# Performance work log

Hardware: AMD Instinct MI355X
Metric: run time of the kernel (lower is better)

## Reference

```python
import jax, jax.numpy as jnp
import numpy as np

B, T, D, N = 256, 512, 512, 64


def setup_inputs() -> dict:
    key = jax.random.key(0)
    ks = jax.random.split(key, 8)
    s = 0.05  # keep gate pre-activations in a sane range
    return {
        "x": jax.random.normal(ks[0], (B, T, D), dtype=jnp.float32),
        "init_h": jax.random.normal(ks[1], (B, D), dtype=jnp.float32) * s,
        "W_ih": jax.random.normal(ks[2], (4 * D, D + N), dtype=jnp.float32) * s,
        "b_ih": jax.random.normal(ks[3], (4 * D,), dtype=jnp.float32) * s,
        "W_hh": jax.random.normal(ks[4], (4 * D, D), dtype=jnp.float32) * s,
        "b_hh": jax.random.normal(ks[5], (4 * D,), dtype=jnp.float32) * s,
        "W_lin": jax.random.normal(ks[6], (N, D), dtype=jnp.float32) * s,
        "b_lin": jax.random.normal(ks[7], (N,), dtype=jnp.float32) * s,
    }


def reference(x, init_h, W_ih, b_ih, W_hh, b_hh, W_lin, b_lin):
    n_class = W_lin.shape[0]
    d = init_h.shape[-1]

    def step(carry, x_t):
        h, c, y = carry
        inp = jnp.concatenate([x_t, y], axis=-1)  # [B, D+N]
        gates = inp @ W_ih.T + b_ih + h @ W_hh.T + b_hh  # [B, 4D]
        i, f, g, o = jnp.split(gates, 4, axis=-1)
        i = jax.nn.sigmoid(i)
        f = jax.nn.sigmoid(f)
        g = jnp.tanh(g)
        o = jax.nn.sigmoid(o)
        c = f * c + i * g
        h = o * jnp.tanh(c)
        y = jax.nn.softmax(h @ W_lin.T + b_lin, axis=-1)  # [B, N]
        return (h, c, y), y

    c0 = jnp.zeros_like(init_h)
    y0 = jnp.zeros((x.shape[0], n_class), dtype=x.dtype)
    xs = jnp.swapaxes(x, 0, 1)  # [T, B, D]
    _, ys = jax.lax.scan(step, (init_h, c0, y0), xs)  # ys: [T, B, N]
    return jnp.swapaxes(ys, 0, 1)  # [B, T, N]
```

## Files before the change

kernel.cpp:

```cpp
#include <hip/hip_runtime.h>
#include <cstdint>
#include <cstddef>


typedef _Float16 f16x8 __attribute__((ext_vector_type(8)));
typedef float f32x4 __attribute__((ext_vector_type(4)));

#define MFMA16(a, b, c_) __builtin_amdgcn_mfma_f32_16x16x32_f16((a), (b), (c_), 0, 0, 0)
#define AGT __HIP_MEMORY_SCOPE_AGENT
#define RLX __ATOMIC_RELAXED

#define FLAG_INTS (256 * 64 + 64)
#define HS2_U32 131072

static __device__ __forceinline__ unsigned short f2b(_Float16 h) {
  return __builtin_bit_cast(unsigned short, h);
}
static __device__ __forceinline__ _Float16 b2f(unsigned short s) {
  return __builtin_bit_cast(_Float16, s);
}

__device__ __forceinline__ void cvt8(const float4 a, const float4 b, f16x8& hi, f16x8& lo) {
  float v[8] = {a.x, a.y, a.z, a.w, b.x, b.y, b.z, b.w};
#pragma unroll
  for (int j = 0; j < 8; ++j) {
    _Float16 h = (_Float16)v[j];
    hi[j] = h;
    lo[j] = (_Float16)(v[j] - (float)h);
  }
}

template <bool XPRE>
__global__ void prep_kernel(const float* __restrict__ x, const float* __restrict__ init_h,
                            const float* __restrict__ W_ih, const float* __restrict__ b_ih,
                            const float* __restrict__ W_hh, const float* __restrict__ b_hh,
                            _Float16* __restrict__ xs, _Float16* __restrict__ wf,
                            unsigned int* __restrict__ hs2, float* __restrict__ bias,
                            int* __restrict__ flags) {
  const long NX = XPRE ? 256L * 512 * 16 * 4 : 0;
  const int NWF = 128 * 34 * 64;
  const int NH2 = 256 * 16 * 4;
  long tid = (long)blockIdx.x * 256 + threadIdx.x;

  if (XPRE && tid < NX) {
    int q = tid & 3, ki = (tid >> 2) & 15, t = (tid >> 6) & 511;
    int row = (int)(tid >> 15);
    const float* s = x + (((size_t)row * 512 + t) * 512 + ki * 32 + 4 * q);
    float4 a = *(const float4*)s, b = *(const float4*)(s + 16);
    f16x8 hi, lo;
    cvt8(a, b, hi, lo);
    _Float16* d = xs + ((((size_t)row * 512 + t) * 16 + ki) * 64 + q * 16);
    *(f16x8*)d = hi;
    *(f16x8*)(d + 8) = lo;
    return;
  }
  long u = tid - NX;
  if (u >= 0 && u < NWF) {
    int l = (int)(u & 63);
    int u2 = (int)(u >> 6);
    int ki = u2 % 34, ct = u2 / 34;
    int cb = ct >> 1, cth = ct & 1;
    int l15 = l & 15;
    int col = (l15 >> 2) * 512 + cb * 8 + cth * 4 + (l15 & 3);
    int k = ki * 32 + 4 * (l >> 4);
    float4 a, b;
    if (k < 512) {
      const float* p = W_ih + (size_t)col * 576;
      a = *(const float4*)(p + k);
      b = *(const float4*)(p + k + 16);
    } else if (k < 1024) {
      const float* p = W_hh + (size_t)col * 512;
      a = *(const float4*)(p + k - 512);
      b = *(const float4*)(p + k - 512 + 16);
    } else {
      const float* p = W_ih + (size_t)col * 576 + 512;
      a = *(const float4*)(p + k - 1024);
      b = *(const float4*)(p + k - 1024 + 16);
    }
    f16x8 hi, lo;
    cvt8(a, b, hi, lo);
    _Float16* d = wf + (((size_t)ct * 34 + ki) * 64 + l) * 16;
    *(f16x8*)d = hi;
    *(f16x8*)(d + 8) = lo;
    return;
  }
  u -= NWF;
  if (u >= 0 && u < NH2) {
    int q = (int)(u & 3), ki = (int)((u >> 2) & 15), row = (int)(u >> 6);
    const float* s = init_h + ((size_t)row * 512 + ki * 32 + 4 * q);
    float4 a = *(const float4*)s, b = *(const float4*)(s + 16);
    float v[8] = {a.x, a.y, a.z, a.w, b.x, b.y, b.z, b.w};
    unsigned int pk[8];
#pragma unroll
    for (int j = 0; j < 8; ++j) {
      _Float16 hh = (_Float16)v[j];
      _Float16 hl = (_Float16)(v[j] - (float)hh);
      pk[j] = (unsigned int)f2b(hh) | ((unsigned int)f2b(hl) << 16);
    }
    unsigned int* base = hs2 + ((size_t)row * 16 + ki) * 32;
    *(uint4*)(base + 4 * q) = make_uint4(pk[0], pk[1], pk[2], pk[3]);
    *(uint4*)(base + 16 + 4 * q) = make_uint4(pk[4], pk[5], pk[6], pk[7]);
    return;
  }
  u -= NH2;
  if (u >= 0 && u < 2048) {
    bias[u] = b_ih[u] + b_hh[u];
    return;
  }
  u -= 2048;
  if (u >= 0 && u < FLAG_INTS) flags[u] = 0;
}

#define GKSTEP(AH, AL, KI)                                                       \
  {                                                                              \
    const f16x8 b0h = *(const f16x8*)(wfl_hi + ((size_t)(KI)*64 + l) * 8);       \
    const f16x8 b1h = *(const f16x8*)(wfl_hi + 17408 + ((size_t)(KI)*64 + l) * 8); \
    const f16x8 b0l = *(const f16x8*)(wfl_lo + ((size_t)(KI)*64 + l) * 8);       \
    const f16x8 b1l = *(const f16x8*)(wfl_lo + 17408 + ((size_t)(KI)*64 + l) * 8); \
    aC0 = MFMA16((AH), b0h, aC0);                                                \
    aC1 = MFMA16((AH), b1h, aC1);                                                \
    aC0 = MFMA16((AL), b0h, aC0);                                                \
    aC1 = MFMA16((AL), b1h, aC1);                                                \
    aC0 = MFMA16((AH), b0l, aC0);                                                \
    aC1 = MFMA16((AH), b1l, aC1);                                                \
  }

template <bool XPRE>
__global__ void __launch_bounds__(512, 2) recur_kernel(
    const float* __restrict__ x, const float* __restrict__ b_lin,
    const float* __restrict__ W_lin, const _Float16* __restrict__ xs,
    const _Float16* __restrict__ wf, unsigned int* __restrict__ hs2,
    const float* __restrict__ bias, float* __restrict__ out, float* __restrict__ ylog,
    int* __restrict__ flags) {
  const int bid = blockIdx.x;
  const int x8 = bid & 7;
  const int g = x8 >> 1;
  const int cb = (x8 & 1) * 32 + (bid >> 3);
  const int tid = threadIdx.x;
  const int l = tid & 63, w = tid >> 6;
  const int l15 = l & 15, q = l >> 4;
  const int kh = w & 1, rtp = w >> 1;

  __shared__ _Float16 wfl_hi[2 * 34 * 64 * 8];
  __shared__ _Float16 wfl_lo[2 * 34 * 64 * 8];
  __shared__ float pacc[4][2][4][64];
  __shared__ float lp[4][16];
  __shared__ int s_ab;

  {
    const _Float16* srcw = wf + (size_t)cb * 4352 * 16;
#pragma unroll
    for (int i = 0; i < 9; ++i) {
      int u = tid + i * 512;
      if (u < 4352) {
        const float4* s16 = (const float4*)(srcw + (size_t)u * 16);
        *(float4*)(wfl_hi + (size_t)u * 8) = s16[0];
        *(float4*)(wfl_lo + (size_t)u * 8) = s16[1];
      }
    }
    if (tid == 0) s_ab = 0;
  }
  __syncthreads();

  const int dd = l15 & 3, rr = l15 >> 2;
  float bg[2][4];
#pragma unroll
  for (int c2 = 0; c2 < 2; ++c2)
#pragma unroll
    for (int gi = 0; gi < 4; ++gi) bg[c2][gi] = bias[gi * 512 + cb * 8 + c2 * 4 + dd];
  const float blin = b_lin[cb];

  const int Rw = g * 64 + rtp * 16;
  const int rowA = Rw + l15;
  const int hoff = rowA * 512 + 4 * q;
  const _Float16* xsA = xs + (size_t)rowA * 524288 + q * 16;
  const float* xfA = x + (size_t)rowA * 262144 + 4 * q;
  const float* wl = W_lin + (size_t)cb * 512;

  const int rowE = Rw + 4 * q + rr;
  unsigned int hwo[2];
#pragma unroll
  for (int c2 = 0; c2 < 2; ++c2) {
    int dglob = cb * 8 + c2 * 4 + dd;
    int kiH = dglob >> 5, k32 = dglob & 31;
    int e = 4 * ((k32 & 15) >> 2) + (k32 & 3) + 16 * (k32 >> 4);
    hwo[c2] = (unsigned int)((rowE * 16 + kiH) * 32 + e);
  }

  int* abortf = flags + 256 * 64;

  auto ARRIVE = [&](int v) {
    __syncthreads();
    if (tid == 0) __hip_atomic_store(flags + (size_t)(g * 64 + cb) * 64, v, RLX, AGT);
  };
  auto WAIT = [&](int v) -> bool {
    if (tid < 64) {
      int a = 0;
      int* f = flags + ((size_t)g * 64 + tid) * 64;
      int it = 0;
      while (__hip_atomic_load(f, RLX, AGT) < v) {
        __builtin_amdgcn_s_sleep(1);
        if (++it > 400000) {
          a = 1;
          break;
        }
        if ((it & 255) == 0 && __hip_atomic_load(abortf, RLX, AGT) != 0) {
          a = 1;
          break;
        }
      }
      a = __any(a) ? 1 : 0;
      if (tid == 0) {
        if (a) __hip_atomic_store(abortf, 1, RLX, AGT);
        s_ab = a;
      }
    }
    __syncthreads();
    return s_ab != 0;
  };

  float cst[2] = {0.f, 0.f};
  f32x4 aC0, aC1;

#pragma unroll 1
  for (int s = 0; s < 512; ++s) {
    aC0 = (f32x4){0.f, 0.f, 0.f, 0.f};
    aC1 = (f32x4){0.f, 0.f, 0.f, 0.f};

    if (XPRE) {
      const _Float16* xA = xsA + (size_t)s * 1024;
#pragma unroll
      for (int i = 0; i < 8; ++i) {
        int kx = kh * 8 + i;
        f16x8 ah = *(const f16x8*)(xA + kx * 64);
        f16x8 al = *(const f16x8*)(xA + kx * 64 + 8);
        GKSTEP(ah, al, kx);
      }
    } else {
      const float* xp = xfA + (size_t)s * 512;
#pragma unroll 2
      for (int i = 0; i < 8; ++i) {
        int kx = kh * 8 + i;
        float4 av = *(const float4*)(xp + kx * 32);
        float4 bv = *(const float4*)(xp + kx * 32 + 16);
        f16x8 ah, al;
        cvt8(av, bv, ah, al);
        GKSTEP(ah, al, kx);
      }
    }

    if (s > 0) {
      if (WAIT(2 * s)) return;
    }

    const unsigned int* hp0 = hs2 + (size_t)(s & 1) * HS2_U32 + hoff;
    f16x8 hh[8], hl[8];
#pragma unroll
    for (int i = 0; i < 8; ++i) {
      const unsigned int* hp = hp0 + (kh * 8 + i) * 32;
      unsigned long long u0 = __hip_atomic_load((const unsigned long long*)hp, RLX, AGT);
      unsigned long long u1 = __hip_atomic_load((const unsigned long long*)(hp + 2), RLX, AGT);
      unsigned long long u2 = __hip_atomic_load((const unsigned long long*)(hp + 16), RLX, AGT);
      unsigned long long u3 = __hip_atomic_load((const unsigned long long*)(hp + 18), RLX, AGT);
      unsigned int wd[8] = {(unsigned int)u0, (unsigned int)(u0 >> 32),
                            (unsigned int)u1, (unsigned int)(u1 >> 32),
                            (unsigned int)u2, (unsigned int)(u2 >> 32),
                            (unsigned int)u3, (unsigned int)(u3 >> 32)};
#pragma unroll
      for (int j = 0; j < 8; ++j) {
        hh[i][j] = b2f((unsigned short)(wd[j] & 0xffffu));
        hl[i][j] = b2f((unsigned short)(wd[j] >> 16));
      }
    }

    float dlg = 0.f;
#pragma unroll
    for (int i = 0; i < 8; ++i) {
      int kk = kh * 8 + i;
      float4 wa = *(const float4*)(wl + kk * 32 + 4 * q);
      float4 wb2 = *(const float4*)(wl + kk * 32 + 16 + 4 * q);
      dlg += ((float)hh[i][0] + (float)hl[i][0]) * wa.x +
             ((float)hh[i][1] + (float)hl[i][1]) * wa.y +
             ((float)hh[i][2] + (float)hl[i][2]) * wa.z +
             ((float)hh[i][3] + (float)hl[i][3]) * wa.w +
             ((float)hh[i][4] + (float)hl[i][4]) * wb2.x +
             ((float)hh[i][5] + (float)hl[i][5]) * wb2.y +
             ((float)hh[i][6] + (float)hl[i][6]) * wb2.z +
             ((float)hh[i][7] + (float)hl[i][7]) * wb2.w;
    }
    dlg += __shfl_xor(dlg, 16);
    dlg += __shfl_xor(dlg, 32);
    if (kh == 1 && l < 16) lp[rtp][l15] = dlg;
    __syncthreads();
    if (kh == 0 && l < 16) {
      float full = dlg + lp[rtp][l15] + blin;
      __hip_atomic_store(ylog + ((size_t)g * 64 + cb) * 64 + rtp * 16 + l15, full, RLX, AGT);
    }
    ARRIVE(2 * s + 1);

#pragma unroll
    for (int i = 0; i < 8; ++i) GKSTEP(hh[i], hl[i], 16 + kh * 8 + i);

    if (WAIT(2 * s + 1)) return;

    if (s > 0) {
      float la[4][4];
#pragma unroll
      for (int b2 = 0; b2 < 4; ++b2)
#pragma unroll
        for (int m = 0; m < 4; ++m)
          la[b2][m] = __hip_atomic_load(
              ylog + ((size_t)g * 64 + 16 * b2 + 4 * q + m) * 64 + rtp * 16 + l15, RLX, AGT);
      float mx = la[0][0];
#pragma unroll
      for (int b2 = 0; b2 < 4; ++b2)
#pragma unroll
        for (int m = 0; m < 4; ++m) mx = fmaxf(mx, la[b2][m]);
      mx = fmaxf(mx, __shfl_xor(mx, 16));
      mx = fmaxf(mx, __shfl_xor(mx, 32));
      float sm = 0.f;
#pragma unroll
      for (int b2 = 0; b2 < 4; ++b2)
#pragma unroll
        for (int m = 0; m < 4; ++m) {
          la[b2][m] = __expf(la[b2][m] - mx);
          sm += la[b2][m];
        }
      sm += __shfl_xor(sm, 16);
      sm += __shfl_xor(sm, 32);
      float inv = 1.f / sm;
      if (cb == 0 && kh == 0) {
        size_t ob = (((size_t)(g * 64 + rtp * 16 + l15)) * 512 + (s - 1)) * 64;
#pragma unroll
        for (int b2 = 0; b2 < 4; ++b2)
#pragma unroll
          for (int m = 0; m < 4; ++m) out[ob + 16 * b2 + 4 * q + m] = la[b2][m] * inv;
      }
      f16x8 yh;
      if (kh == 0) {
#pragma unroll
        for (int j = 0; j < 8; ++j) yh[j] = (_Float16)(la[j >> 2][j & 3] * inv);
      } else {
#pragma unroll
        for (int j = 0; j < 8; ++j) yh[j] = (_Float16)(la[(j >> 2) + 2][j & 3] * inv);
      }
      const int KY = 32 + kh;
      const f16x8 b0h = *(const f16x8*)(wfl_hi + ((size_t)KY * 64 + l) * 8);
      const f16x8 b1h = *(const f16x8*)(wfl_hi + 17408 + ((size_t)KY * 64 + l) * 8);
      const f16x8 b0l = *(const f16x8*)(wfl_lo + ((size_t)KY * 64 + l) * 8);
      const f16x8 b1l = *(const f16x8*)(wfl_lo + 17408 + ((size_t)KY * 64 + l) * 8);
      aC0 = MFMA16(yh, b0h, aC0);
      aC1 = MFMA16(yh, b1h, aC1);
      aC0 = MFMA16(yh, b0l, aC0);
      aC1 = MFMA16(yh, b1l, aC1);
    }

    if (kh == 1) {
#pragma unroll
      for (int r = 0; r < 4; ++r) {
        pacc[rtp][0][r][l] = aC0[r];
        pacc[rtp][1][r][l] = aC1[r];
      }
    }
    __syncthreads();
    if (kh == 0) {
#pragma unroll
      for (int r = 0; r < 4; ++r) {
        aC0[r] += pacc[rtp][0][r][l];
        aC1[r] += pacc[rtp][1][r][l];
      }
      const unsigned int wb_ = (unsigned int)(((s & 1) ^ 1) * HS2_U32);
#pragma unroll
      for (int c2 = 0; c2 < 2; ++c2) {
        f32x4 A = c2 ? aC1 : aC0;
        float z[4];
#pragma unroll
        for (int gi = 0; gi < 4; ++gi) {
          int src = (l & 48) | (gi * 4 + dd);
          float v0 = __shfl(A[0], src), v1 = __shfl(A[1], src);
          float v2 = __shfl(A[2], src), v3 = __shfl(A[3], src);
          z[gi] = (rr == 0) ? v0 : (rr == 1) ? v1 : (rr == 2) ? v2 : v3;
        }
        float zi = z[0] + bg[c2][0], zf = z[1] + bg[c2][1];
        float zg = z[2] + bg[c2][2], zo = z[3] + bg[c2][3];
        float iv = 1.f / (1.f + __expf(-zi));
        float fv = 1.f / (1.f + __expf(-zf));
        float eg = __expf(2.f * zg);
        float gv = 1.f - 2.f / (eg + 1.f);
        float ov = 1.f / (1.f + __expf(-zo));
        float cn = fv * cst[c2] + iv * gv;
        cst[c2] = cn;
        float ec = __expf(2.f * cn);
        float th = 1.f - 2.f / (ec + 1.f);
        float hv = ov * th;
        _Float16 hh2 = (_Float16)hv;
        _Float16 hl2 = (_Float16)(hv - (float)hh2);
        unsigned int pk = (unsigned int)f2b(hh2) | ((unsigned int)f2b(hl2) << 16);
        __hip_atomic_store(hs2 + wb_ + hwo[c2], pk, RLX, AGT);
      }
    }
    ARRIVE(2 * s + 2);
  }

  if (WAIT(1024)) return;
  {
    const unsigned int* hp0 = hs2 + hoff;
    float dlg = 0.f;
#pragma unroll
    for (int i = 0; i < 8; ++i) {
      int kk = kh * 8 + i;
      const unsigned int* hp = hp0 + kk * 32;
      unsigned long long u0 = __hip_atomic_load((const unsigned long long*)hp, RLX, AGT);
      unsigned long long u1 = __hip_atomic_load((const unsigned long long*)(hp + 2), RLX, AGT);
      unsigned long long u2 = __hip_atomic_load((const unsigned long long*)(hp + 16), RLX, AGT);
      unsigned long long u3 = __hip_atomic_load((const unsigned long long*)(hp + 18), RLX, AGT);
      unsigned int wd[8] = {(unsigned int)u0, (unsigned int)(u0 >> 32),
                            (unsigned int)u1, (unsigned int)(u1 >> 32),
                            (unsigned int)u2, (unsigned int)(u2 >> 32),
                            (unsigned int)u3, (unsigned int)(u3 >> 32)};
      float4 wa = *(const float4*)(wl + kk * 32 + 4 * q);
      float4 wb2 = *(const float4*)(wl + kk * 32 + 16 + 4 * q);
      float hv0[8];
#pragma unroll
      for (int j = 0; j < 8; ++j)
        hv0[j] = (float)b2f((unsigned short)(wd[j] & 0xffffu)) +
                 (float)b2f((unsigned short)(wd[j] >> 16));
      dlg += hv0[0] * wa.x + hv0[1] * wa.y + hv0[2] * wa.z + hv0[3] * wa.w + hv0[4] * wb2.x +
             hv0[5] * wb2.y + hv0[6] * wb2.z + hv0[7] * wb2.w;
    }
    dlg += __shfl_xor(dlg, 16);
    dlg += __shfl_xor(dlg, 32);
    if (kh == 1 && l < 16) lp[rtp][l15] = dlg;
    __syncthreads();
    if (kh == 0 && l < 16)
      __hip_atomic_store(ylog + ((size_t)g * 64 + cb) * 64 + rtp * 16 + l15,
                         dlg + lp[rtp][l15] + blin, RLX, AGT);
  }
  ARRIVE(1025);
  if (WAIT(1025)) return;
  if (cb == 0 && kh == 0) {
    float la[4][4];
#pragma unroll
    for (int b2 = 0; b2 < 4; ++b2)
#pragma unroll
      for (int m = 0; m < 4; ++m)
        la[b2][m] = __hip_atomic_load(
            ylog + ((size_t)g * 64 + 16 * b2 + 4 * q + m) * 64 + rtp * 16 + l15, RLX, AGT);
    float mx = la[0][0];
#pragma unroll
    for (int b2 = 0; b2 < 4; ++b2)
#pragma unroll
      for (int m = 0; m < 4; ++m) mx = fmaxf(mx, la[b2][m]);
    mx = fmaxf(mx, __shfl_xor(mx, 16));
    mx = fmaxf(mx, __shfl_xor(mx, 32));
    float sm = 0.f;
#pragma unroll
    for (int b2 = 0; b2 < 4; ++b2)
#pragma unroll
      for (int m = 0; m < 4; ++m) {
        la[b2][m] = __expf(la[b2][m] - mx);
        sm += la[b2][m];
      }
    sm += __shfl_xor(sm, 16);
    sm += __shfl_xor(sm, 32);
    float inv = 1.f / sm;
    size_t ob = (((size_t)(g * 64 + rtp * 16 + l15)) * 512 + 511) * 64;
#pragma unroll
    for (int b2 = 0; b2 < 4; ++b2)
#pragma unroll
      for (int m = 0; m < 4; ++m) out[ob + 16 * b2 + 4 * q + m] = la[b2][m] * inv;
  }
}

extern "C" void kernel_launch(void* const* d_in, const int* in_sizes, int n_in, void* d_out,
                              int out_size, void* d_ws, size_t ws_size, hipStream_t stream) {
  const float* x = (const float*)d_in[0];
  const float* init_h = (const float*)d_in[1];
  const float* W_ih = (const float*)d_in[2];
  const float* b_ih = (const float*)d_in[3];
  const float* W_hh = (const float*)d_in[4];
  const float* b_hh = (const float*)d_in[5];
  const float* W_lin = (const float*)d_in[6];
  const float* b_lin = (const float*)d_in[7];
  float* out = (float*)d_out;
  (void)in_sizes;
  (void)n_in;
  (void)out_size;

  char* ws = (char*)d_ws;
  size_t off = 0;
  auto take = [&](size_t bytes) -> char* {
    char* r = ws + off;
    off = (off + bytes + 255) & ~(size_t)255;
    return r;
  };
  const size_t WF_E = (size_t)128 * 34 * 64 * 16;
  const size_t XS_E = (size_t)256 * 512 * 16 * 64;

  _Float16* wf = (_Float16*)take(WF_E * 2);
  unsigned int* hs2 = (unsigned int*)take((size_t)2 * HS2_U32 * 4);
  float* bias = (float*)take(2048 * 4);
  float* ylogb = (float*)take((size_t)4 * 64 * 64 * 4);
  int* flags = (int*)take((size_t)FLAG_INTS * 4);
  if (ws_size < off) return;
  _Float16* xs = (_Float16*)(ws + off);
  const bool xpre = (ws_size >= off + XS_E * 2);

  if (xpre) {
    const long total = 8388608L + 278528 + 16384 + 2048 + FLAG_INTS;
    prep_kernel<true><<<(int)((total + 255) / 256), 256, 0, stream>>>(
        x, init_h, W_ih, b_ih, W_hh, b_hh, xs, wf, hs2, bias, flags);
    recur_kernel<true><<<256, 512, 0, stream>>>(x, b_lin, W_lin, xs, wf, hs2, bias, out, ylogb,
                                                flags);
  } else {
    const long total = 278528L + 16384 + 2048 + FLAG_INTS;
    prep_kernel<false><<<(int)((total + 255) / 256), 256, 0, stream>>>(
        x, init_h, W_ih, b_ih, W_hh, b_hh, xs, wf, hs2, bias, flags);
    recur_kernel<false><<<256, 512, 0, stream>>>(x, b_lin, W_lin, xs, wf, hs2, bias, out, ylogb,
                                                 flags);
  }
}
```

Before: 8.857 ms.

## Compute output logits redundantly per block via MFMA, halving grid barriers per step

Each block now computes the full 64-class logit projection and softmax for its rows with MFMA, using an hi/lo fp16 copy of W_lin kept in LDS. This removes the second cross-block barrier and the shared logit buffer per timestep. The gate weights are no longer staged in LDS and are read from global memory instead. The x-projection for the next step is issued after the arrive so it can overlap the barrier wait. In exchange the linear layer is computed redundantly in every column block, and all gate-weight traffic now goes through the global cache.

```diff
diff --git a/kernel.cpp b/kernel.cpp
--- a/kernel.cpp
+++ b/kernel.cpp
@@ -5,6 +5,7 @@
 
 typedef _Float16 f16x8 __attribute__((ext_vector_type(8)));
 typedef float f32x4 __attribute__((ext_vector_type(4)));
+typedef unsigned long long u64;
 
 #define MFMA16(a, b, c_) __builtin_amdgcn_mfma_f32_16x16x32_f16((a), (b), (c_), 0, 0, 0)
 #define AGT __HIP_MEMORY_SCOPE_AGENT
@@ -34,12 +35,14 @@
 __global__ void prep_kernel(const float* __restrict__ x, const float* __restrict__ init_h,
                             const float* __restrict__ W_ih, const float* __restrict__ b_ih,
                             const float* __restrict__ W_hh, const float* __restrict__ b_hh,
-                            _Float16* __restrict__ xs, _Float16* __restrict__ wf,
-                            unsigned int* __restrict__ hs2, float* __restrict__ bias,
-                            int* __restrict__ flags) {
+                            const float* __restrict__ W_lin, _Float16* __restrict__ xs,
+                            _Float16* __restrict__ wf, _Float16* __restrict__ wlf_hi,
+                            _Float16* __restrict__ wlf_lo, unsigned int* __restrict__ hs2,
+                            float* __restrict__ bias, int* __restrict__ flags) {
   const long NX = XPRE ? 256L * 512 * 16 * 4 : 0;
   const int NWF = 128 * 34 * 64;
-  const int NH2 = 256 * 16 * 4;
+  const int NWLF = 4 * 16 * 64;
+  const int NH2 = 256 * 128;
   long tid = (long)blockIdx.x * 256 + threadIdx.x;
 
   if (XPRE && tid < NX) {
@@ -85,21 +88,35 @@
     return;
   }
   u -= NWF;
+  if (u >= 0 && u < NWLF) {
+    int l = (int)(u & 63);
+    int u2 = (int)(u >> 6);
+    int ki = u2 & 15, ct = u2 >> 4;
+    int col = ct * 16 + (l & 15);
+    int k = ki * 32 + 4 * (l >> 4);
+    const float* p = W_lin + (size_t)col * 512;
+    float4 a = *(const float4*)(p + k), b = *(const float4*)(p + k + 16);
+    f16x8 hi, lo;
+    cvt8(a, b, hi, lo);
+    _Float16* dh = wlf_hi + ((size_t)(ct * 16 + ki) * 64 + l) * 8;
+    _Float16* dl = wlf_lo + ((size_t)(ct * 16 + ki) * 64 + l) * 8;
+    *(f16x8*)dh = hi;
+    *(f16x8*)dl = lo;
+    return;
+  }
+  u -= NWLF;
   if (u >= 0 && u < NH2) {
-    int q = (int)(u & 3), ki = (int)((u >> 2) & 15), row = (int)(u >> 6);
-    const float* s = init_h + ((size_t)row * 512 + ki * 32 + 4 * q);
-    float4 a = *(const float4*)s, b = *(const float4*)(s + 16);
-    float v[8] = {a.x, a.y, a.z, a.w, b.x, b.y, b.z, b.w};
-    unsigned int pk[8];
-#pragma unroll
-    for (int j = 0; j < 8; ++j) {
+    int g4 = (int)(u & 127), row = (int)(u >> 7);
+    const float* s = init_h + (size_t)row * 512 + g4 * 4;
+    float4 a = *(const float4*)s;
+    float v[4] = {a.x, a.y, a.z, a.w};
+    unsigned int* d = hs2 + (size_t)row * 512 + g4 * 4;
+#pragma unroll
+    for (int j = 0; j < 4; ++j) {
       _Float16 hh = (_Float16)v[j];
       _Float16 hl = (_Float16)(v[j] - (float)hh);
-      pk[j] = (unsigned int)f2b(hh) | ((unsigned int)f2b(hl) << 16);
-    }
-    unsigned int* base = hs2 + ((size_t)row * 16 + ki) * 32;
-    *(uint4*)(base + 4 * q) = make_uint4(pk[0], pk[1], pk[2], pk[3]);
-    *(uint4*)(base + 16 + 4 * q) = make_uint4(pk[4], pk[5], pk[6], pk[7]);
+      d[j] = (unsigned int)f2b(hh) | ((unsigned int)f2b(hl) << 16);
+    }
     return;
   }
   u -= NH2;
@@ -111,26 +128,12 @@
   if (u >= 0 && u < FLAG_INTS) flags[u] = 0;
 }
 
-#define GKSTEP(AH, AL, KI)                                                       \
-  {                                                                              \
-    const f16x8 b0h = *(const f16x8*)(wfl_hi + ((size_t)(KI)*64 + l) * 8);       \
-    const f16x8 b1h = *(const f16x8*)(wfl_hi + 17408 + ((size_t)(KI)*64 + l) * 8); \
-    const f16x8 b0l = *(const f16x8*)(wfl_lo + ((size_t)(KI)*64 + l) * 8);       \
-    const f16x8 b1l = *(const f16x8*)(wfl_lo + 17408 + ((size_t)(KI)*64 + l) * 8); \
-    aC0 = MFMA16((AH), b0h, aC0);                                                \
-    aC1 = MFMA16((AH), b1h, aC1);                                                \
-    aC0 = MFMA16((AL), b0h, aC0);                                                \
-    aC1 = MFMA16((AL), b1h, aC1);                                                \
-    aC0 = MFMA16((AH), b0l, aC0);                                                \
-    aC1 = MFMA16((AH), b1l, aC1);                                                \
-  }
-
 template <bool XPRE>
-__global__ void __launch_bounds__(512, 2) recur_kernel(
+__global__ void __launch_bounds__(512, 1) recur_kernel(
     const float* __restrict__ x, const float* __restrict__ b_lin,
-    const float* __restrict__ W_lin, const _Float16* __restrict__ xs,
-    const _Float16* __restrict__ wf, unsigned int* __restrict__ hs2,
-    const float* __restrict__ bias, float* __restrict__ out, float* __restrict__ ylog,
+    const _Float16* __restrict__ xs, const _Float16* __restrict__ wf,
+    const _Float16* __restrict__ wlf_hi, const _Float16* __restrict__ wlf_lo,
+    unsigned int* __restrict__ hs2, const float* __restrict__ bias, float* __restrict__ out,
     int* __restrict__ flags) {
   const int bid = blockIdx.x;
   const int x8 = bid & 7;
@@ -141,22 +144,17 @@
   const int l15 = l & 15, q = l >> 4;
   const int kh = w & 1, rtp = w >> 1;
 
-  __shared__ _Float16 wfl_hi[2 * 34 * 64 * 8];
-  __shared__ _Float16 wfl_lo[2 * 34 * 64 * 8];
-  __shared__ float pacc[4][2][4][64];
-  __shared__ float lp[4][16];
+  __shared__ _Float16 wlin_h[4 * 16 * 64 * 8];
+  __shared__ _Float16 wlin_l[4 * 16 * 64 * 8];
+  __shared__ float scratch[4608];
   __shared__ int s_ab;
 
   {
-    const _Float16* srcw = wf + (size_t)cb * 4352 * 16;
-#pragma unroll
-    for (int i = 0; i < 9; ++i) {
+#pragma unroll
+    for (int i = 0; i < 8; ++i) {
       int u = tid + i * 512;
-      if (u < 4352) {
-        const float4* s16 = (const float4*)(srcw + (size_t)u * 16);
-        *(float4*)(wfl_hi + (size_t)u * 8) = s16[0];
-        *(float4*)(wfl_lo + (size_t)u * 8) = s16[1];
-      }
+      *(float4*)(wlin_h + (size_t)u * 8) = *(const float4*)(wlf_hi + (size_t)u * 8);
+      *(float4*)(wlin_l + (size_t)u * 8) = *(const float4*)(wlf_lo + (size_t)u * 8);
     }
     if (tid == 0) s_ab = 0;
   }
@@ -168,24 +166,17 @@
   for (int c2 = 0; c2 < 2; ++c2)
 #pragma unroll
     for (int gi = 0; gi < 4; ++gi) bg[c2][gi] = bias[gi * 512 + cb * 8 + c2 * 4 + dd];
-  const float blin = b_lin[cb];
+  const float blv0 = b_lin[l15], blv1 = b_lin[16 + l15];
+  const float blv2 = b_lin[32 + l15], blv3 = b_lin[48 + l15];
 
   const int Rw = g * 64 + rtp * 16;
   const int rowA = Rw + l15;
-  const int hoff = rowA * 512 + 4 * q;
   const _Float16* xsA = xs + (size_t)rowA * 524288 + q * 16;
   const float* xfA = x + (size_t)rowA * 262144 + 4 * q;
-  const float* wl = W_lin + (size_t)cb * 512;
-
+  const unsigned int* hldA = hs2 + (size_t)rowA * 512 + 4 * q;
   const int rowE = Rw + 4 * q + rr;
-  unsigned int hwo[2];
-#pragma unroll
-  for (int c2 = 0; c2 < 2; ++c2) {
-    int dglob = cb * 8 + c2 * 4 + dd;
-    int kiH = dglob >> 5, k32 = dglob & 31;
-    int e = 4 * ((k32 & 15) >> 2) + (k32 & 3) + 16 * (k32 >> 4);
-    hwo[c2] = (unsigned int)((rowE * 16 + kiH) * 32 + e);
-  }
+
+  const _Float16* wfb = wf + ((size_t)(2 * cb) * 34) * 1024 + (size_t)l * 16;
 
   int* abortf = flags + 256 * 64;
 
@@ -219,25 +210,30 @@
     return s_ab != 0;
   };
 
-  float cst[2] = {0.f, 0.f};
-  f32x4 aC0, aC1;
-
-#pragma unroll 1
-  for (int s = 0; s < 512; ++s) {
-    aC0 = (f32x4){0.f, 0.f, 0.f, 0.f};
-    aC1 = (f32x4){0.f, 0.f, 0.f, 0.f};
-
+  auto GK3 = [&](const f16x8& ah, const f16x8& al, int KI, f32x4& A0, f32x4& A1) {
+    const _Float16* p0 = wfb + (size_t)KI * 1024;
+    const _Float16* p1 = p0 + 34 * 1024;
+    f16x8 b0h = *(const f16x8*)p0, b0l = *(const f16x8*)(p0 + 8);
+    f16x8 b1h = *(const f16x8*)p1, b1l = *(const f16x8*)(p1 + 8);
+    A0 = MFMA16(ah, b0h, A0);
+    A1 = MFMA16(ah, b1h, A1);
+    A0 = MFMA16(al, b0h, A0);
+    A1 = MFMA16(al, b1h, A1);
+    A0 = MFMA16(ah, b0l, A0);
+    A1 = MFMA16(ah, b1l, A1);
+  };
+  auto XGEMM = [&](int t, f32x4& A0, f32x4& A1) {
     if (XPRE) {
-      const _Float16* xA = xsA + (size_t)s * 1024;
+      const _Float16* xA = xsA + (size_t)t * 1024;
 #pragma unroll
       for (int i = 0; i < 8; ++i) {
         int kx = kh * 8 + i;
         f16x8 ah = *(const f16x8*)(xA + kx * 64);
         f16x8 al = *(const f16x8*)(xA + kx * 64 + 8);
-        GKSTEP(ah, al, kx);
+        GK3(ah, al, kx, A0, A1);
       }
     } else {
-      const float* xp = xfA + (size_t)s * 512;
+      const float* xp = xfA + (size_t)t * 512;
 #pragma unroll 2
       for (int i = 0; i < 8; ++i) {
         int kx = kh * 8 + i;
@@ -245,23 +241,31 @@
         float4 bv = *(const float4*)(xp + kx * 32 + 16);
         f16x8 ah, al;
         cvt8(av, bv, ah, al);
-        GKSTEP(ah, al, kx);
-      }
-    }
-
+        GK3(ah, al, kx, A0, A1);
+      }
+    }
+  };
+
+  const f32x4 Z = {0.f, 0.f, 0.f, 0.f};
+  float cst[2] = {0.f, 0.f};
+  f32x4 aC0 = Z, aC1 = Z;
+  XGEMM(0, aC0, aC1);
+
+#pragma unroll 1
+  for (int s = 0; s < 512; ++s) {
     if (s > 0) {
-      if (WAIT(2 * s)) return;
-    }
-
-    const unsigned int* hp0 = hs2 + (size_t)(s & 1) * HS2_U32 + hoff;
+      if (WAIT(s)) return;
+    }
+
     f16x8 hh[8], hl[8];
+    const unsigned int* hp0 = hldA + (size_t)(s & 1) * HS2_U32;
 #pragma unroll
     for (int i = 0; i < 8; ++i) {
       const unsigned int* hp = hp0 + (kh * 8 + i) * 32;
-      unsigned long long u0 = __hip_atomic_load((const unsigned long long*)hp, RLX, AGT);
-      unsigned long long u1 = __hip_atomic_load((const unsigned long long*)(hp + 2), RLX, AGT);
-      unsigned long long u2 = __hip_atomic_load((const unsigned long long*)(hp + 16), RLX, AGT);
-      unsigned long long u3 = __hip_atomic_load((const unsigned long long*)(hp + 18), RLX, AGT);
+      u64 u0 = __hip_atomic_load((const u64*)hp, RLX, AGT);
+      u64 u1 = __hip_atomic_load((const u64*)(hp + 2), RLX, AGT);
+      u64 u2 = __hip_atomic_load((const u64*)(hp + 16), RLX, AGT);
+      u64 u3 = __hip_atomic_load((const u64*)(hp + 18), RLX, AGT);
       unsigned int wd[8] = {(unsigned int)u0, (unsigned int)(u0 >> 32),
                             (unsigned int)u1, (unsigned int)(u1 >> 32),
                             (unsigned int)u2, (unsigned int)(u2 >> 32),
@@ -273,103 +277,137 @@
       }
     }
 
-    float dlg = 0.f;
-#pragma unroll
-    for (int i = 0; i < 8; ++i) {
-      int kk = kh * 8 + i;
-      float4 wa = *(const float4*)(wl + kk * 32 + 4 * q);
-      float4 wb2 = *(const float4*)(wl + kk * 32 + 16 + 4 * q);
-      dlg += ((float)hh[i][0] + (float)hl[i][0]) * wa.x +
-             ((float)hh[i][1] + (float)hl[i][1]) * wa.y +
-             ((float)hh[i][2] + (float)hl[i][2]) * wa.z +
-             ((float)hh[i][3] + (float)hl[i][3]) * wa.w +
-             ((float)hh[i][4] + (float)hl[i][4]) * wb2.x +
-             ((float)hh[i][5] + (float)hl[i][5]) * wb2.y +
-             ((float)hh[i][6] + (float)hl[i][6]) * wb2.z +
-             ((float)hh[i][7] + (float)hl[i][7]) * wb2.w;
-    }
-    dlg += __shfl_xor(dlg, 16);
-    dlg += __shfl_xor(dlg, 32);
-    if (kh == 1 && l < 16) lp[rtp][l15] = dlg;
-    __syncthreads();
-    if (kh == 0 && l < 16) {
-      float full = dlg + lp[rtp][l15] + blin;
-      __hip_atomic_store(ylog + ((size_t)g * 64 + cb) * 64 + rtp * 16 + l15, full, RLX, AGT);
-    }
-    ARRIVE(2 * s + 1);
-
-#pragma unroll
-    for (int i = 0; i < 8; ++i) GKSTEP(hh[i], hl[i], 16 + kh * 8 + i);
-
-    if (WAIT(2 * s + 1)) return;
-
+    f32x4 y0 = Z, y1 = Z, y2 = Z, y3 = Z;
     if (s > 0) {
-      float la[4][4];
-#pragma unroll
-      for (int b2 = 0; b2 < 4; ++b2)
-#pragma unroll
-        for (int m = 0; m < 4; ++m)
-          la[b2][m] = __hip_atomic_load(
-              ylog + ((size_t)g * 64 + 16 * b2 + 4 * q + m) * 64 + rtp * 16 + l15, RLX, AGT);
-      float mx = la[0][0];
-#pragma unroll
-      for (int b2 = 0; b2 < 4; ++b2)
-#pragma unroll
-        for (int m = 0; m < 4; ++m) mx = fmaxf(mx, la[b2][m]);
-      mx = fmaxf(mx, __shfl_xor(mx, 16));
-      mx = fmaxf(mx, __shfl_xor(mx, 32));
-      float sm = 0.f;
-#pragma unroll
-      for (int b2 = 0; b2 < 4; ++b2)
-#pragma unroll
-        for (int m = 0; m < 4; ++m) {
-          la[b2][m] = __expf(la[b2][m] - mx);
-          sm += la[b2][m];
-        }
-      sm += __shfl_xor(sm, 16);
-      sm += __shfl_xor(sm, 32);
-      float inv = 1.f / sm;
-      if (cb == 0 && kh == 0) {
-        size_t ob = (((size_t)(g * 64 + rtp * 16 + l15)) * 512 + (s - 1)) * 64;
-#pragma unroll
-        for (int b2 = 0; b2 < 4; ++b2)
-#pragma unroll
-          for (int m = 0; m < 4; ++m) out[ob + 16 * b2 + 4 * q + m] = la[b2][m] * inv;
-      }
-      f16x8 yh;
+#pragma unroll
+      for (int i = 0; i < 8; ++i) {
+        int ki = kh * 8 + i;
+        const _Float16* ph0 = wlin_h + ((size_t)(0 * 16 + ki) * 64 + l) * 8;
+        const _Float16* ph1 = wlin_h + ((size_t)(1 * 16 + ki) * 64 + l) * 8;
+        const _Float16* ph2 = wlin_h + ((size_t)(2 * 16 + ki) * 64 + l) * 8;
+        const _Float16* ph3 = wlin_h + ((size_t)(3 * 16 + ki) * 64 + l) * 8;
+        f16x8 b0 = *(const f16x8*)ph0, b1 = *(const f16x8*)ph1;
+        f16x8 b2 = *(const f16x8*)ph2, b3 = *(const f16x8*)ph3;
+        y0 = MFMA16(hh[i], b0, y0);
+        y1 = MFMA16(hh[i], b1, y1);
+        y2 = MFMA16(hh[i], b2, y2);
+        y3 = MFMA16(hh[i], b3, y3);
+        y0 = MFMA16(hl[i], b0, y0);
+        y1 = MFMA16(hl[i], b1, y1);
+        y2 = MFMA16(hl[i], b2, y2);
+        y3 = MFMA16(hl[i], b3, y3);
+        const _Float16* pl0 = wlin_l + ((size_t)(0 * 16 + ki) * 64 + l) * 8;
+        const _Float16* pl1 = wlin_l + ((size_t)(1 * 16 + ki) * 64 + l) * 8;
+        const _Float16* pl2 = wlin_l + ((size_t)(2 * 16 + ki) * 64 + l) * 8;
+        const _Float16* pl3 = wlin_l + ((size_t)(3 * 16 + ki) * 64 + l) * 8;
+        f16x8 c0 = *(const f16x8*)pl0, c1 = *(const f16x8*)pl1;
+        f16x8 c2v = *(const f16x8*)pl2, c3 = *(const f16x8*)pl3;
+        y0 = MFMA16(hh[i], c0, y0);
+        y1 = MFMA16(hh[i], c1, y1);
+        y2 = MFMA16(hh[i], c2v, y2);
+        y3 = MFMA16(hh[i], c3, y3);
+      }
+    }
+#pragma unroll
+    for (int i = 0; i < 8; ++i) GK3(hh[i], hl[i], 16 + kh * 8 + i, aC0, aC1);
+
+    if (s > 0) {
+      if (kh == 1) {
+#pragma unroll
+        for (int r = 0; r < 4; ++r) {
+          scratch[((rtp * 4 + 0) * 4 + r) * 64 + l] = y0[r];
+          scratch[((rtp * 4 + 1) * 4 + r) * 64 + l] = y1[r];
+          scratch[((rtp * 4 + 2) * 4 + r) * 64 + l] = y2[r];
+          scratch[((rtp * 4 + 3) * 4 + r) * 64 + l] = y3[r];
+        }
+      }
+      __syncthreads();
+      float la0[4], la1[4], la2[4], la3[4];
       if (kh == 0) {
 #pragma unroll
-        for (int j = 0; j < 8; ++j) yh[j] = (_Float16)(la[j >> 2][j & 3] * inv);
-      } else {
-#pragma unroll
-        for (int j = 0; j < 8; ++j) yh[j] = (_Float16)(la[(j >> 2) + 2][j & 3] * inv);
-      }
-      const int KY = 32 + kh;
-      const f16x8 b0h = *(const f16x8*)(wfl_hi + ((size_t)KY * 64 + l) * 8);
-      const f16x8 b1h = *(const f16x8*)(wfl_hi + 17408 + ((size_t)KY * 64 + l) * 8);
-      const f16x8 b0l = *(const f16x8*)(wfl_lo + ((size_t)KY * 64 + l) * 8);
-      const f16x8 b1l = *(const f16x8*)(wfl_lo + 17408 + ((size_t)KY * 64 + l) * 8);
-      aC0 = MFMA16(yh, b0h, aC0);
-      aC1 = MFMA16(yh, b1h, aC1);
-      aC0 = MFMA16(yh, b0l, aC0);
-      aC1 = MFMA16(yh, b1l, aC1);
+        for (int r = 0; r < 4; ++r) {
+          la0[r] = y0[r] + scratch[((rtp * 4 + 0) * 4 + r) * 64 + l] + blv0;
+          la1[r] = y1[r] + scratch[((rtp * 4 + 1) * 4 + r) * 64 + l] + blv1;
+          la2[r] = y2[r] + scratch[((rtp * 4 + 2) * 4 + r) * 64 + l] + blv2;
+          la3[r] = y3[r] + scratch[((rtp * 4 + 3) * 4 + r) * 64 + l] + blv3;
+        }
+#pragma unroll
+        for (int r = 0; r < 4; ++r) {
+          float mx = fmaxf(fmaxf(la0[r], la1[r]), fmaxf(la2[r], la3[r]));
+          mx = fmaxf(mx, __shfl_xor(mx, 1));
+          mx = fmaxf(mx, __shfl_xor(mx, 2));
+          mx = fmaxf(mx, __shfl_xor(mx, 4));
+          mx = fmaxf(mx, __shfl_xor(mx, 8));
+          float e0 = __expf(la0[r] - mx), e1 = __expf(la1[r] - mx);
+          float e2 = __expf(la2[r] - mx), e3 = __expf(la3[r] - mx);
+          float sm = e0 + e1 + e2 + e3;
+          sm += __shfl_xor(sm, 1);
+          sm += __shfl_xor(sm, 2);
+          sm += __shfl_xor(sm, 4);
+          sm += __shfl_xor(sm, 8);
+          float inv = 1.f / sm;
+          la0[r] = e0 * inv;
+          la1[r] = e1 * inv;
+          la2[r] = e2 * inv;
+          la3[r] = e3 * inv;
+        }
+        if (cb == 0) {
+#pragma unroll
+          for (int r = 0; r < 4; ++r) {
+            size_t ob = ((size_t)(g * 64 + rtp * 16 + 4 * q + r) * 512 + (s - 1)) * 64 + l15;
+            out[ob] = la0[r];
+            out[ob + 16] = la1[r];
+            out[ob + 32] = la2[r];
+            out[ob + 48] = la3[r];
+          }
+        }
+      }
+      __syncthreads();
+      if (kh == 0) {
+        _Float16* yt = (_Float16*)scratch;
+#pragma unroll
+        for (int r = 0; r < 4; ++r) {
+          int row = rtp * 16 + 4 * q + r;
+          float v[4] = {la0[r], la1[r], la2[r], la3[r]};
+#pragma unroll
+          for (int ct = 0; ct < 4; ++ct) {
+            _Float16 vh = (_Float16)v[ct];
+            _Float16 vl = (_Float16)(v[ct] - (float)vh);
+            yt[row * 136 + ct * 16 + l15] = vh;
+            yt[row * 136 + 72 + ct * 16 + l15] = vl;
+          }
+        }
+      }
+      __syncthreads();
+      {
+        const _Float16* yt = (const _Float16*)scratch + (rtp * 16 + l15) * 136 + kh * 32 + 4 * q;
+        union {
+          u64 d[2];
+          f16x8 v;
+        } th, tl;
+        th.d[0] = *(const u64*)yt;
+        th.d[1] = *(const u64*)(yt + 16);
+        tl.d[0] = *(const u64*)(yt + 72);
+        tl.d[1] = *(const u64*)(yt + 88);
+        GK3(th.v, tl.v, 32 + kh, aC0, aC1);
+      }
+      __syncthreads();
     }
 
     if (kh == 1) {
 #pragma unroll
       for (int r = 0; r < 4; ++r) {
-        pacc[rtp][0][r][l] = aC0[r];
-        pacc[rtp][1][r][l] = aC1[r];
+        scratch[((rtp * 2 + 0) * 4 + r) * 64 + l] = aC0[r];
+        scratch[((rtp * 2 + 1) * 4 + r) * 64 + l] = aC1[r];
       }
     }
     __syncthreads();
     if (kh == 0) {
 #pragma unroll
       for (int r = 0; r < 4; ++r) {
-        aC0[r] += pacc[rtp][0][r][l];
-        aC1[r] += pacc[rtp][1][r][l];
-      }
-      const unsigned int wb_ = (unsigned int)(((s & 1) ^ 1) * HS2_U32);
+        aC0[r] += scratch[((rtp * 2 + 0) * 4 + r) * 64 + l];
+        aC1[r] += scratch[((rtp * 2 + 1) * 4 + r) * 64 + l];
+      }
 #pragma unroll
       for (int c2 = 0; c2 < 2; ++c2) {
         f32x4 A = c2 ? aC1 : aC0;
@@ -391,84 +429,117 @@
         float cn = fv * cst[c2] + iv * gv;
         cst[c2] = cn;
         float ec = __expf(2.f * cn);
-        float th = 1.f - 2.f / (ec + 1.f);
-        float hv = ov * th;
-        _Float16 hh2 = (_Float16)hv;
-        _Float16 hl2 = (_Float16)(hv - (float)hh2);
-        unsigned int pk = (unsigned int)f2b(hh2) | ((unsigned int)f2b(hl2) << 16);
-        __hip_atomic_store(hs2 + wb_ + hwo[c2], pk, RLX, AGT);
-      }
-    }
-    ARRIVE(2 * s + 2);
-  }
-
-  if (WAIT(1024)) return;
+        float th2 = 1.f - 2.f / (ec + 1.f);
+        float hv = ov * th2;
+        _Float16 hhv = (_Float16)hv;
+        _Float16 hlv = (_Float16)(hv - (float)hhv);
+        unsigned int pk = (unsigned int)f2b(hhv) | ((unsigned int)f2b(hlv) << 16);
+        int dglob = cb * 8 + c2 * 4 + dd;
+        __hip_atomic_store(hs2 + (size_t)((s + 1) & 1) * HS2_U32 + rowE * 512 + dglob, pk, RLX,
+                           AGT);
+      }
+    }
+    ARRIVE(s + 1);
+    if (s < 511) {
+      f32x4 aN0 = Z, aN1 = Z;
+      XGEMM(s + 1, aN0, aN1);
+      aC0 = aN0;
+      aC1 = aN1;
+    }
+  }
+
+  if (cb != 0) return;
+  if (WAIT(512)) return;
   {
-    const unsigned int* hp0 = hs2 + hoff;
-    float dlg = 0.f;
+    f16x8 hh[8], hl[8];
+    const unsigned int* hp0 = hldA;
 #pragma unroll
     for (int i = 0; i < 8; ++i) {
-      int kk = kh * 8 + i;
-      const unsigned int* hp = hp0 + kk * 32;
-      unsigned long long u0 = __hip_atomic_load((const unsigned long long*)hp, RLX, AGT);
-      unsigned long long u1 = __hip_atomic_load((const unsigned long long*)(hp + 2), RLX, AGT);
-      unsigned long long u2 = __hip_atomic_load((const unsigned long long*)(hp + 16), RLX, AGT);
-      unsigned long long u3 = __hip_atomic_load((const unsigned long long*)(hp + 18), RLX, AGT);
+      const unsigned int* hp = hp0 + (kh * 8 + i) * 32;
+      u64 u0 = __hip_atomic_load((const u64*)hp, RLX, AGT);
+      u64 u1 = __hip_atomic_load((const u64*)(hp + 2), RLX, AGT);
+      u64 u2 = __hip_atomic_load((const u64*)(hp + 16), RLX, AGT);
+      u64 u3 = __hip_atomic_load((const u64*)(hp + 18), RLX, AGT);
       unsigned int wd[8] = {(unsigned int)u0, (unsigned int)(u0 >> 32),
                             (unsigned int)u1, (unsigned int)(u1 >> 32),
                             (unsigned int)u2, (unsigned int)(u2 >> 32),
                             (unsigned int)u3, (unsigned int)(u3 >> 32)};
-      float4 wa = *(const float4*)(wl + kk * 32 + 4 * q);
-      float4 wb2 = *(const float4*)(wl + kk * 32 + 16 + 4 * q);
-      float hv0[8];
-#pragma unroll
-      for (int j = 0; j < 8; ++j)
-        hv0[j] = (float)b2f((unsigned short)(wd[j] & 0xffffu)) +
-                 (float)b2f((unsigned short)(wd[j] >> 16));
-      dlg += hv0[0] * wa.x + hv0[1] * wa.y + hv0[2] * wa.z + hv0[3] * wa.w + hv0[4] * wb2.x +
-             hv0[5] * wb2.y + hv0[6] * wb2.z + hv0[7] * wb2.w;
-    }
-    dlg += __shfl_xor(dlg, 16);
-    dlg += __shfl_xor(dlg, 32);
-    if (kh == 1 && l < 16) lp[rtp][l15] = dlg;
+#pragma unroll
+      for (int j = 0; j < 8; ++j) {
+        hh[i][j] = b2f((unsigned short)(wd[j] & 0xffffu));
+        hl[i][j] = b2f((unsigned short)(wd[j] >> 16));
+      }
+    }
+    f32x4 y0 = Z, y1 = Z, y2 = Z, y3 = Z;
+#pragma unroll
+    for (int i = 0; i < 8; ++i) {
+      int ki = kh * 8 + i;
+      const _Float16* ph0 = wlin_h + ((size_t)(0 * 16 + ki) * 64 + l) * 8;
+      const _Float16* ph1 = wlin_h + ((size_t)(1 * 16 + ki) * 64 + l) * 8;
+      const _Float16* ph2 = wlin_h + ((size_t)(2 * 16 + ki) * 64 + l) * 8;
+      const _Float16* ph3 = wlin_h + ((size_t)(3 * 16 + ki) * 64 + l) * 8;
+      f16x8 b0 = *(const f16x8*)ph0, b1 = *(const f16x8*)ph1;
+      f16x8 b2 = *(const f16x8*)ph2, b3 = *(const f16x8*)ph3;
+      y0 = MFMA16(hh[i], b0, y0);
+      y1 = MFMA16(hh[i], b1, y1);
+      y2 = MFMA16(hh[i], b2, y2);
+      y3 = MFMA16(hh[i], b3, y3);
+      y0 = MFMA16(hl[i], b0, y0);
+      y1 = MFMA16(hl[i], b1, y1);
+      y2 = MFMA16(hl[i], b2, y2);
+      y3 = MFMA16(hl[i], b3, y3);
+      const _Float16* pl0 = wlin_l + ((size_t)(0 * 16 + ki) * 64 + l) * 8;
+      const _Float16* pl1 = wlin_l + ((size_t)(1 * 16 + ki) * 64 + l) * 8;
+      const _Float16* pl2 = wlin_l + ((size_t)(2 * 16 + ki) * 64 + l) * 8;
+      const _Float16* pl3 = wlin_l + ((size_t)(3 * 16 + ki) * 64 + l) * 8;
+      f16x8 c0 = *(const f16x8*)pl0, c1 = *(const f16x8*)pl1;
+      f16x8 c2v = *(const f16x8*)pl2, c3 = *(const f16x8*)pl3;
+      y0 = MFMA16(hh[i], c0, y0);
+      y1 = MFMA16(hh[i], c1, y1);
+      y2 = MFMA16(hh[i], c2v, y2);
+      y3 = MFMA16(hh[i], c3, y3);
+    }
+    if (kh == 1) {
+#pragma unroll
+      for (int r = 0; r < 4; ++r) {
+        scratch[((rtp * 4 + 0) * 4 + r) * 64 + l] = y0[r];
+        scratch[((rtp * 4 + 1) * 4 + r) * 64 + l] = y1[r];
+        scratch[((rtp * 4 + 2) * 4 + r) * 64 + l] = y2[r];
+        scratch[((rtp * 4 + 3) * 4 + r) * 64 + l] = y3[r];
+      }
+    }
     __syncthreads();
-    if (kh == 0 && l < 16)
-      __hip_atomic_store(ylog + ((size_t)g * 64 + cb) * 64 + rtp * 16 + l15,
-                         dlg + lp[rtp][l15] + blin, RLX, AGT);
-  }
-  ARRIVE(1025);
-  if (WAIT(1025)) return;
-  if (cb == 0 && kh == 0) {
-    float la[4][4];
-#pragma unroll
-    for (int b2 = 0; b2 < 4; ++b2)
-#pragma unroll
-      for (int m = 0; m < 4; ++m)
-        la[b2][m] = __hip_atomic_load(
-            ylog + ((size_t)g * 64 + 16 * b2 + 4 * q + m) * 64 + rtp * 16 + l15, RLX, AGT);
-    float mx = la[0][0];
-#pragma unroll
-    for (int b2 = 0; b2 < 4; ++b2)
-#pragma unroll
-      for (int m = 0; m < 4; ++m) mx = fmaxf(mx, la[b2][m]);
-    mx = fmaxf(mx, __shfl_xor(mx, 16));
-    mx = fmaxf(mx, __shfl_xor(mx, 32));
-    float sm = 0.f;
-#pragma unroll
-    for (int b2 = 0; b2 < 4; ++b2)
-#pragma unroll
-      for (int m = 0; m < 4; ++m) {
-        la[b2][m] = __expf(la[b2][m] - mx);
-        sm += la[b2][m];
-      }
-    sm += __shfl_xor(sm, 16);
-    sm += __shfl_xor(sm, 32);
-    float inv = 1.f / sm;
-    size_t ob = (((size_t)(g * 64 + rtp * 16 + l15)) * 512 + 511) * 64;
-#pragma unroll
-    for (int b2 = 0; b2 < 4; ++b2)
-#pragma unroll
-      for (int m = 0; m < 4; ++m) out[ob + 16 * b2 + 4 * q + m] = la[b2][m] * inv;
+    if (kh == 0) {
+      float la0[4], la1[4], la2[4], la3[4];
+#pragma unroll
+      for (int r = 0; r < 4; ++r) {
+        la0[r] = y0[r] + scratch[((rtp * 4 + 0) * 4 + r) * 64 + l] + blv0;
+        la1[r] = y1[r] + scratch[((rtp * 4 + 1) * 4 + r) * 64 + l] + blv1;
+        la2[r] = y2[r] + scratch[((rtp * 4 + 2) * 4 + r) * 64 + l] + blv2;
+        la3[r] = y3[r] + scratch[((rtp * 4 + 3) * 4 + r) * 64 + l] + blv3;
+      }
+#pragma unroll
+      for (int r = 0; r < 4; ++r) {
+        float mx = fmaxf(fmaxf(la0[r], la1[r]), fmaxf(la2[r], la3[r]));
+        mx = fmaxf(mx, __shfl_xor(mx, 1));
+        mx = fmaxf(mx, __shfl_xor(mx, 2));
+        mx = fmaxf(mx, __shfl_xor(mx, 4));
+        mx = fmaxf(mx, __shfl_xor(mx, 8));
+        float e0 = __expf(la0[r] - mx), e1 = __expf(la1[r] - mx);
+        float e2 = __expf(la2[r] - mx), e3 = __expf(la3[r] - mx);
+        float sm = e0 + e1 + e2 + e3;
+        sm += __shfl_xor(sm, 1);
+        sm += __shfl_xor(sm, 2);
+        sm += __shfl_xor(sm, 4);
+        sm += __shfl_xor(sm, 8);
+        float inv = 1.f / sm;
+        size_t ob = ((size_t)(g * 64 + rtp * 16 + 4 * q + r) * 512 + 511) * 64 + l15;
+        out[ob] = e0 * inv;
+        out[ob + 16] = e1 * inv;
+        out[ob + 32] = e2 * inv;
+        out[ob + 48] = e3 * inv;
+      }
+    }
   }
 }
 
@@ -495,28 +566,30 @@
     return r;
   };
   const size_t WF_E = (size_t)128 * 34 * 64 * 16;
+  const size_t WLF_E = (size_t)4 * 16 * 64 * 8;
   const size_t XS_E = (size_t)256 * 512 * 16 * 64;
 
   _Float16* wf = (_Float16*)take(WF_E * 2);
+  _Float16* wlf_hi = (_Float16*)take(WLF_E * 2);
+  _Float16* wlf_lo = (_Float16*)take(WLF_E * 2);
   unsigned int* hs2 = (unsigned int*)take((size_t)2 * HS2_U32 * 4);
   float* bias = (float*)take(2048 * 4);
-  float* ylogb = (float*)take((size_t)4 * 64 * 64 * 4);
   int* flags = (int*)take((size_t)FLAG_INTS * 4);
   if (ws_size < off) return;
   _Float16* xs = (_Float16*)(ws + off);
   const bool xpre = (ws_size >= off + XS_E * 2);
 
   if (xpre) {
-    const long total = 8388608L + 278528 + 16384 + 2048 + FLAG_INTS;
+    const long total = 8388608L + 278528 + 4096 + 32768 + 2048 + FLAG_INTS;
     prep_kernel<true><<<(int)((total + 255) / 256), 256, 0, stream>>>(
-        x, init_h, W_ih, b_ih, W_hh, b_hh, xs, wf, hs2, bias, flags);
-    recur_kernel<true><<<256, 512, 0, stream>>>(x, b_lin, W_lin, xs, wf, hs2, bias, out, ylogb,
+        x, init_h, W_ih, b_ih, W_hh, b_hh, W_lin, xs, wf, wlf_hi, wlf_lo, hs2, bias, flags);
+    recur_kernel<true><<<256, 512, 0, stream>>>(x, b_lin, xs, wf, wlf_hi, wlf_lo, hs2, bias, out,
                                                 flags);
   } else {
-    const long total = 278528L + 16384 + 2048 + FLAG_INTS;
+    const long total = 278528L + 4096 + 32768 + 2048 + FLAG_INTS;
     prep_kernel<false><<<(int)((total + 255) / 256), 256, 0, stream>>>(
-        x, init_h, W_ih, b_ih, W_hh, b_hh, xs, wf, hs2, bias, flags);
-    recur_kernel<false><<<256, 512, 0, stream>>>(x, b_lin, W_lin, xs, wf, hs2, bias, out, ylogb,
+        x, init_h, W_ih, b_ih, W_hh, b_hh, W_lin, xs, wf, wlf_hi, wlf_lo, hs2, bias, flags);
+    recur_kernel<false><<<256, 512, 0, stream>>>(x, b_lin, xs, wf, wlf_hi, wlf_lo, hs2, bias, out,
                                                  flags);
   }
 }
```

Result: slower. 13.78 ms (+55.5%).
